# Kernel optimization log

Hardware: AMD Instinct MI355X
Metric: run time of the kernel (lower is better)

Reference implementation:

```python
import jax, jax.numpy as jnp
import numpy as np

BN_EPS = 1e-5
NN_EPS = 1e-8


def _conv_bn_relu(x, w, gamma, beta, mean, var):
    # x: (B, Cin, N), w: (Cout, Cin) -- 1x1 Conv1d (no bias) + BatchNorm1d (eval) + ReLU
    y = jnp.einsum('oc,bcn->bon', w, x)
    scale = gamma / jnp.sqrt(var + BN_EPS)            # (Cout,)
    shift = beta - mean * scale                       # (Cout,)
    return jax.nn.relu(y * scale[:, None] + shift[:, None])


def setup_inputs() -> dict:
    key = jax.random.key(0)
    ks = jax.random.split(key, 10)
    B, N, M = 4, 2048, 8192
    Cin, Cout = 512, 256
    inp = {
        'x1': jax.random.normal(ks[0], (B, Cin, N), dtype=jnp.float32),
        'p1': jax.random.uniform(ks[1], (B, N, 3), dtype=jnp.float32) * 4.0,
        'x2': jax.random.normal(ks[2], (B, Cout, M), dtype=jnp.float32),
        'p2': jax.random.uniform(ks[3], (B, M, 3), dtype=jnp.float32) * 4.0,
        # up_mlp params
        'w_up': jax.random.normal(ks[4], (Cout, Cin), dtype=jnp.float32) * (1.0 / np.sqrt(Cin)),
        'g_up': jnp.ones((Cout,), jnp.float32),
        'b_up': jnp.zeros((Cout,), jnp.float32),
        'm_up': jax.random.normal(ks[5], (Cout,), dtype=jnp.float32) * 0.1,
        'v_up': jax.random.uniform(ks[6], (Cout,), dtype=jnp.float32) + 0.5,
        # lateral_mlp params
        'w_lat': jax.random.normal(ks[7], (Cout, Cout), dtype=jnp.float32) * (1.0 / np.sqrt(Cout)),
        'g_lat': jnp.ones((Cout,), jnp.float32),
        'b_lat': jnp.zeros((Cout,), jnp.float32),
        'm_lat': jax.random.normal(ks[8], (Cout,), dtype=jnp.float32) * 0.1,
        'v_lat': jax.random.uniform(ks[9], (Cout,), dtype=jnp.float32) + 0.5,
    }
    return inp


def reference(x1, p1, x2, p2, w_up, g_up, b_up, m_up, v_up,
              w_lat, g_lat, b_lat, m_lat, v_lat):
    # up branch: conv1x1 + BN + ReLU on coarse features  (B, Cout, N)
    f1 = _conv_bn_relu(x1, w_up, g_up, b_up, m_up, v_up)

    # three_nn: for each fine point p2 find 3 nearest coarse points p1 (squared dist)
    d2 = (jnp.sum(p2 * p2, -1)[:, :, None]
          + jnp.sum(p1 * p1, -1)[:, None, :]
          - 2.0 * jnp.einsum('bmd,bnd->bmn', p2, p1))        # (B, M, N)
    d2 = jnp.maximum(d2, 0.0)
    neg_d, idx = jax.lax.top_k(-d2, 3)                       # (B, M, 3)
    dist = -neg_d

    # inverse-distance weights
    dist_recip = 1.0 / (dist + NN_EPS)
    weight = dist_recip / jnp.sum(dist_recip, axis=2, keepdims=True)  # (B, M, 3)

    # three_interpolate: gather + weighted sum
    gathered = jax.vmap(lambda f, i: f[:, i])(f1, idx)       # (B, Cout, M, 3)
    interp = jnp.einsum('bcmk,bmk->bcm', gathered, weight)   # (B, Cout, M)

    # lateral branch
    f2 = _conv_bn_relu(x2, w_lat, g_lat, b_lat, m_lat, v_lat)

    return interp + f2, p2
```

## Files before the change

kernel.cpp:

```cpp
#include <hip/hip_runtime.h>
#include <math.h>
#include <float.h>

#define B_    4
#define N_    2048
#define M_    8192
#define CIN_  512
#define COUT_ 256

typedef __attribute__((ext_vector_type(8))) short short8v;
typedef __attribute__((ext_vector_type(4))) float f32x4;

__device__ __forceinline__ void ws_store_f32(float* p, float v) {
    __hip_atomic_store((unsigned int*)p, __float_as_uint(v),
                       __ATOMIC_RELAXED, __HIP_MEMORY_SCOPE_SYSTEM);
}
__device__ __forceinline__ void ws_store_u32(int* p, int v) {
    __hip_atomic_store((unsigned int*)p, (unsigned int)v,
                       __ATOMIC_RELAXED, __HIP_MEMORY_SCOPE_SYSTEM);
}
__device__ __forceinline__ void l2_invalidate() {
    asm volatile("buffer_inv sc0 sc1" ::: "memory");
}

__device__ __forceinline__ unsigned short f2bf(float f) {
    unsigned u = __float_as_uint(f);
    u += 0x7fffu + ((u >> 16) & 1u);
    return (unsigned short)(u >> 16);
}

template<int K, int MODE>
__device__ __forceinline__ void gemm_body(
    char* raw, int b, int c0, int m0,
    const float* __restrict__ X, const float* __restrict__ W,
    const float* __restrict__ gam, const float* __restrict__ bet,
    const float* __restrict__ mu, const float* __restrict__ var,
    float* __restrict__ dst,
    const float* __restrict__ f1t, const int* __restrict__ nn_idx,
    const float* __restrict__ nn_w, int Mdim)
{
    char* Ab = raw;
    char* Bb = raw + 10240;

    const int tid = threadIdx.x;
    const int l  = tid & 63;
    const int wv = tid >> 6;
    const int wc = wv & 1, wn = wv >> 1;

    f32x4 acc[4][4];
    #pragma unroll
    for (int i = 0; i < 4; ++i)
        #pragma unroll
        for (int j = 0; j < 4; ++j)
            acc[i][j] = (f32x4){0.f, 0.f, 0.f, 0.f};

    const int ksA = tid & 7;
    const int crA = tid >> 3;
    const int kqB = tid >> 5;
    const int mlB = tid & 31;

    for (int kc = 0; kc < K; kc += 32) {
        #pragma unroll
        for (int r = 0; r < 4; ++r) {
            int c = crA + 32 * r;
            float4 v = *(const float4*)(W + (size_t)(c0 + c) * K + kc + ksA * 4);
            unsigned lo = f2bf(v.x) | ((unsigned)f2bf(v.y) << 16);
            unsigned hi = f2bf(v.z) | ((unsigned)f2bf(v.w) << 16);
            *(uint2*)(Ab + c * 80 + ksA * 8) = make_uint2(lo, hi);
        }
        #pragma unroll
        for (int jj = 0; jj < 4; ++jj) {
            int m = mlB + 32 * jj;
            const float* xp = X + ((size_t)b * K + kc + kqB * 4) * Mdim + m0 + m;
            float v0 = xp[0];
            float v1 = xp[(size_t)Mdim];
            float v2 = xp[(size_t)2 * Mdim];
            float v3 = xp[(size_t)3 * Mdim];
            unsigned lo = f2bf(v0) | ((unsigned)f2bf(v1) << 16);
            unsigned hi = f2bf(v2) | ((unsigned)f2bf(v3) << 16);
            *(uint2*)(Bb + m * 80 + kqB * 8) = make_uint2(lo, hi);
        }
        __syncthreads();
        short8v a[4], bf[4];
        #pragma unroll
        for (int ci = 0; ci < 4; ++ci)
            a[ci] = *(const short8v*)(Ab + (wc * 64 + ci * 16 + (l & 15)) * 80 + (l >> 4) * 16);
        #pragma unroll
        for (int ni = 0; ni < 4; ++ni)
            bf[ni] = *(const short8v*)(Bb + (wn * 64 + ni * 16 + (l & 15)) * 80 + (l >> 4) * 16);
        #pragma unroll
        for (int ci = 0; ci < 4; ++ci)
            #pragma unroll
            for (int ni = 0; ni < 4; ++ni)
                acc[ci][ni] = __builtin_amdgcn_mfma_f32_16x16x32_bf16(
                    a[ci], bf[ni], acc[ci][ni], 0, 0, 0);
        __syncthreads();
    }

    const int lc = (l >> 4) * 4;
    float scA[4][4], shA[4][4];
    #pragma unroll
    for (int ci = 0; ci < 4; ++ci)
        #pragma unroll
        for (int r = 0; r < 4; ++r) {
            int c = c0 + wc * 64 + ci * 16 + lc + r;
            float sc = gam[c] / sqrtf(var[c] + 1e-5f);
            scA[ci][r] = sc;
            shA[ci][r] = bet[c] - mu[c] * sc;
        }

    if constexpr (MODE == 0) {
        float* S = (float*)raw;
        #pragma unroll
        for (int h = 0; h < 2; ++h) {
            if (wn == h) {
                #pragma unroll
                for (int ni = 0; ni < 4; ++ni)
                    #pragma unroll
                    for (int ci = 0; ci < 4; ++ci)
                        #pragma unroll
                        for (int r = 0; r < 4; ++r)
                            S[(ni * 16 + (l & 15)) * 133 + wc * 64 + ci * 16 + lc + r] =
                                fmaxf(acc[ci][ni][r] * scA[ci][r] + shA[ci][r], 0.f);
            }
            __syncthreads();
            #pragma unroll
            for (int i = 0; i < 32; ++i) {
                int e = tid + i * 256;
                int row = e >> 7, c = e & 127;
                ws_store_f32(dst + ((size_t)b * N_ + m0 + h * 64 + row) * COUT_ + c0 + c,
                             S[row * 133 + c]);
            }
            __syncthreads();
        }
    } else {
        #pragma unroll
        for (int ni = 0; ni < 4; ++ni) {
            int mg = m0 + wn * 64 + ni * 16 + (l & 15);
            size_t io = ((size_t)b * M_ + mg) * 3;
            int   i0 = nn_idx[io + 0];
            int   i1 = nn_idx[io + 1];
            int   i2 = nn_idx[io + 2];
            float w0 = nn_w[io + 0];
            float w1 = nn_w[io + 1];
            float w2 = nn_w[io + 2];
            const float4* g0 = (const float4*)(f1t + ((size_t)b * N_ + i0) * COUT_ + c0 + wc * 64 + lc);
            const float4* g1 = (const float4*)(f1t + ((size_t)b * N_ + i1) * COUT_ + c0 + wc * 64 + lc);
            const float4* g2 = (const float4*)(f1t + ((size_t)b * N_ + i2) * COUT_ + c0 + wc * 64 + lc);
            #pragma unroll
            for (int ci = 0; ci < 4; ++ci) {
                float4 G0 = g0[ci * 4];
                float4 G1 = g1[ci * 4];
                float4 G2 = g2[ci * 4];
                const float* f0 = (const float*)&G0;
                const float* f1 = (const float*)&G1;
                const float* f2 = (const float*)&G2;
                #pragma unroll
                for (int r = 0; r < 4; ++r) {
                    float v = fmaxf(acc[ci][ni][r] * scA[ci][r] + shA[ci][r], 0.f);
                    v = fmaf(w0, f0[r], v);
                    v = fmaf(w1, f1[r], v);
                    v = fmaf(w2, f2[r], v);
                    int c = c0 + wc * 64 + ci * 16 + lc + r;
                    dst[((size_t)b * COUT_ + c) * M_ + mg] = v;
                }
            }
        }
    }
}

__device__ __forceinline__ void lex_insert(float e, int j,
    float& D0, float& D1, float& D2, int& I0, int& I1, int& I2)
{
    bool l0 = (e < D0) || (e == D0 && j < I0);
    bool l1 = (e < D1) || (e == D1 && j < I1);
    bool l2 = (e < D2) || (e == D2 && j < I2);
    if (l2) {
        if (l0)      { D2=D1; I2=I1; D1=D0; I1=I0; D0=e; I0=j; }
        else if (l1) { D2=D1; I2=I1; D1=e;  I1=j; }
        else         { D2=e;  I2=j; }
    }
}

__device__ __forceinline__ void bubble_insert(float e, int ie,
    float& D0, float& D1, float& D2, int& I0, int& I1, int& I2)
{
    bool l2 = e < D2;
    D2 = l2 ? e  : D2;
    I2 = l2 ? ie : I2;
    bool s1 = D2 < D1;
    float tf = D1; int ti = I1;
    D1 = s1 ? D2 : D1;  I1 = s1 ? I2 : I1;
    D2 = s1 ? tf : D2;  I2 = s1 ? ti : I2;
    bool s0 = D1 < D0;
    tf = D0; ti = I0;
    D0 = s0 ? D1 : D0;  I0 = s0 ? I1 : I0;
    D1 = s0 ? tf : D1;  I1 = s0 ? ti : I1;
}

__device__ __forceinline__ void three_nn_body(
    float4 (*P)[257], int b, int mb,
    const float* __restrict__ p1, const float* __restrict__ p2,
    int* __restrict__ nn_idx, float* __restrict__ nn_w,
    float* __restrict__ out1)
{
    #pragma unroll
    for (int r = 0; r < 8; ++r) {
        int n = r * 256 + threadIdx.x;
        float x = p1[((size_t)(b*N_)+n)*3 + 0];
        float y = p1[((size_t)(b*N_)+n)*3 + 1];
        float z = p1[((size_t)(b*N_)+n)*3 + 2];
        float t = x * x;
        t = fmaf(y, y, t);
        t = fmaf(z, z, t);
        P[r][threadIdx.x] = make_float4(x, y, z, t);
    }
    __syncthreads();

    const int m = mb * 32 + (threadIdx.x >> 3);
    const int s = threadIdx.x & 7;
    const size_t pbase = ((size_t)(b*M_) + m) * 3;
    const float qx = p2[pbase+0], qy = p2[pbase+1], qz = p2[pbase+2];
    float s2 = qx * qx;
    s2 = fmaf(qy, qy, s2);
    s2 = fmaf(qz, qz, s2);

    float D0 = FLT_MAX, D1 = FLT_MAX, D2 = FLT_MAX;
    int   I0 = 0x7fffffff, I1 = 0x7fffffff, I2 = 0x7fffffff;
    const int base = s * 256;
    const float4* Ps = &P[s][0];

    for (int t = 0; t < 256; t += 8) {
        float4 c[8];
        #pragma unroll
        for (int u = 0; u < 8; ++u) c[u] = Ps[t + u];
        float d[8];
        #pragma unroll
        for (int u = 0; u < 8; ++u) {
            float dot = qx * c[u].x;
            dot = fmaf(qy, c[u].y, dot);
            dot = fmaf(qz, c[u].z, dot);
            float d2 = fmaf(-2.0f, dot, s2 + c[u].w);
            d[u] = fmaxf(d2, 0.0f);
        }
        #pragma unroll
        for (int u = 0; u < 8; ++u)
            bubble_insert(d[u], base + t + u, D0, D1, D2, I0, I1, I2);
    }

    #pragma unroll
    for (int st = 1; st <= 4; st <<= 1) {
        float E0 = __shfl_xor(D0, st), E1 = __shfl_xor(D1, st), E2 = __shfl_xor(D2, st);
        int   J0 = __shfl_xor(I0, st), J1 = __shfl_xor(I1, st), J2 = __shfl_xor(I2, st);
        lex_insert(E0, J0, D0, D1, D2, I0, I1, I2);
        lex_insert(E1, J1, D0, D1, D2, I0, I1, I2);
        lex_insert(E2, J2, D0, D1, D2, I0, I1, I2);
    }
    if (s == 0) {
        float r0 = 1.0f / (D0 + 1e-8f);
        float r1 = 1.0f / (D1 + 1e-8f);
        float r2 = 1.0f / (D2 + 1e-8f);
        float sum = (r0 + r1) + r2;
        size_t o = ((size_t)(b*M_) + m) * 3;
        ws_store_u32(nn_idx + o+0, I0);
        ws_store_u32(nn_idx + o+1, I1);
        ws_store_u32(nn_idx + o+2, I2);
        ws_store_f32(nn_w + o+0, r0 / sum);
        ws_store_f32(nn_w + o+1, r1 / sum);
        ws_store_f32(nn_w + o+2, r2 / sum);
        out1[o+0] = qx; out1[o+1] = qy; out1[o+2] = qz;
    }
}

__global__ __launch_bounds__(256) void up_nn_kernel(
    const float* __restrict__ x1, const float* __restrict__ w_up,
    const float* __restrict__ g_up, const float* __restrict__ b_up,
    const float* __restrict__ m_up, const float* __restrict__ v_up,
    float* __restrict__ f1t,
    const float* __restrict__ p1, const float* __restrict__ p2,
    int* __restrict__ nn_idx, float* __restrict__ nn_w,
    float* __restrict__ out1)
{
    __shared__ float4 raw4[2130];
    int bid = blockIdx.x;
    if (bid < 128) {
        int nb = bid & 15, cb = (bid >> 4) & 1, b = bid >> 5;
        gemm_body<CIN_, 0>((char*)raw4, b, cb * 128, nb * 128,
                           x1, w_up, g_up, b_up, m_up, v_up, f1t,
                           nullptr, nullptr, nullptr, N_);
    } else {
        int v = bid - 128;
        int mb = v & 255, b = v >> 8;
        three_nn_body((float4(*)[257])raw4, b, mb, p1, p2, nn_idx, nn_w, out1);
    }
}

__global__ __launch_bounds__(256) void lat_kernel(
    const float* __restrict__ x2, const float* __restrict__ w_lat,
    const float* __restrict__ g_lat, const float* __restrict__ b_lat,
    const float* __restrict__ m_lat, const float* __restrict__ v_lat,
    const float* __restrict__ f1t, const int* __restrict__ nn_idx,
    const float* __restrict__ nn_w, float* __restrict__ out0)
{
    __shared__ float4 raw4[1280];
    l2_invalidate();
    gemm_body<COUT_, 1>((char*)raw4, blockIdx.z, blockIdx.y * 128, blockIdx.x * 128,
                        x2, w_lat, g_lat, b_lat, m_lat, v_lat, out0,
                        f1t, nn_idx, nn_w, M_);
}

extern "C" void kernel_launch(void* const* d_in, const int* in_sizes, int n_in,
                              void* d_out, int out_size, void* d_ws, size_t ws_size,
                              hipStream_t stream)
{
    (void)in_sizes; (void)n_in; (void)out_size; (void)ws_size;

    const float* x1    = (const float*)d_in[0];
    const float* p1    = (const float*)d_in[1];
    const float* x2    = (const float*)d_in[2];
    const float* p2    = (const float*)d_in[3];
    const float* w_up  = (const float*)d_in[4];
    const float* g_up  = (const float*)d_in[5];
    const float* b_up  = (const float*)d_in[6];
    const float* m_up  = (const float*)d_in[7];
    const float* v_up  = (const float*)d_in[8];
    const float* w_lat = (const float*)d_in[9];
    const float* g_lat = (const float*)d_in[10];
    const float* b_lat = (const float*)d_in[11];
    const float* m_lat = (const float*)d_in[12];
    const float* v_lat = (const float*)d_in[13];

    float* out0 = (float*)d_out;
    float* out1 = out0 + (size_t)B_ * COUT_ * M_;

    float* f1t   = (float*)d_ws;
    int*   nn_idx = (int*)((char*)d_ws + (size_t)B_ * N_ * COUT_ * 4);
    float* nn_w   = (float*)((char*)nn_idx + (size_t)B_ * M_ * 3 * 4);

    up_nn_kernel<<<dim3(128 + 1024), 256, 0, stream>>>(
        x1, w_up, g_up, b_up, m_up, v_up, f1t, p1, p2, nn_idx, nn_w, out1);

    lat_kernel<<<dim3(M_ / 128, COUT_ / 128, B_), 256, 0, stream>>>(
        x2, w_lat, g_lat, b_lat, m_lat, v_lat, f1t, nn_idx, nn_w, out0);
}
```

Baseline: 115.4 us.

## Split fused up/NN kernel, prefetch GEMM tiles in registers, pack NN records

Splits the fused up-projection plus three_nn kernel into separate launches and adds a dedicated cache-invalidate kernel in place of the per-block invalidate in lat_kernel. The GEMM body now loads the next K-slice into registers while the current one is converted and stored to shared memory, to hide global load latency. The three_nn inner loop double-buffers LDS reads. Neighbor indices and weights are packed into one 8-float record per point, so the lateral kernel fetches them with two vector loads. The extra launches add overhead and remove the overlap that the fused kernel had between the GEMM and the NN search.

```diff
diff --git a/kernel.cpp b/kernel.cpp
--- a/kernel.cpp
+++ b/kernel.cpp
@@ -19,7 +19,8 @@
     __hip_atomic_store((unsigned int*)p, (unsigned int)v,
                        __ATOMIC_RELAXED, __HIP_MEMORY_SCOPE_SYSTEM);
 }
-__device__ __forceinline__ void l2_invalidate() {
+
+__global__ __launch_bounds__(64) void inv_kernel() {
     asm volatile("buffer_inv sc0 sc1" ::: "memory");
 }
 
@@ -36,8 +37,7 @@
     const float* __restrict__ gam, const float* __restrict__ bet,
     const float* __restrict__ mu, const float* __restrict__ var,
     float* __restrict__ dst,
-    const float* __restrict__ f1t, const int* __restrict__ nn_idx,
-    const float* __restrict__ nn_w, int Mdim)
+    const float* __restrict__ f1t, const float* __restrict__ nnrec, int Mdim)
 {
     char* Ab = raw;
     char* Bb = raw + 10240;
@@ -59,41 +59,60 @@
     const int kqB = tid >> 5;
     const int mlB = tid & 31;
 
+    float4 wreg[4];
+    float  xreg[4][4];
+    #pragma unroll
+    for (int r = 0; r < 4; ++r)
+        wreg[r] = *(const float4*)(W + (size_t)(c0 + crA + 32 * r) * K + ksA * 4);
+    #pragma unroll
+    for (int jj = 0; jj < 4; ++jj) {
+        const float* xp = X + ((size_t)b * K + kqB * 4) * Mdim + m0 + mlB + 32 * jj;
+        xreg[jj][0] = xp[0];
+        xreg[jj][1] = xp[(size_t)Mdim];
+        xreg[jj][2] = xp[(size_t)2 * Mdim];
+        xreg[jj][3] = xp[(size_t)3 * Mdim];
+    }
+
     for (int kc = 0; kc < K; kc += 32) {
         #pragma unroll
         for (int r = 0; r < 4; ++r) {
-            int c = crA + 32 * r;
-            float4 v = *(const float4*)(W + (size_t)(c0 + c) * K + kc + ksA * 4);
-            unsigned lo = f2bf(v.x) | ((unsigned)f2bf(v.y) << 16);
-            unsigned hi = f2bf(v.z) | ((unsigned)f2bf(v.w) << 16);
-            *(uint2*)(Ab + c * 80 + ksA * 8) = make_uint2(lo, hi);
+            unsigned lo = f2bf(wreg[r].x) | ((unsigned)f2bf(wreg[r].y) << 16);
+            unsigned hi = f2bf(wreg[r].z) | ((unsigned)f2bf(wreg[r].w) << 16);
+            *(uint2*)(Ab + (crA + 32 * r) * 80 + ksA * 8) = make_uint2(lo, hi);
         }
         #pragma unroll
         for (int jj = 0; jj < 4; ++jj) {
-            int m = mlB + 32 * jj;
-            const float* xp = X + ((size_t)b * K + kc + kqB * 4) * Mdim + m0 + m;
-            float v0 = xp[0];
-            float v1 = xp[(size_t)Mdim];
-            float v2 = xp[(size_t)2 * Mdim];
-            float v3 = xp[(size_t)3 * Mdim];
-            unsigned lo = f2bf(v0) | ((unsigned)f2bf(v1) << 16);
-            unsigned hi = f2bf(v2) | ((unsigned)f2bf(v3) << 16);
-            *(uint2*)(Bb + m * 80 + kqB * 8) = make_uint2(lo, hi);
+            unsigned lo = f2bf(xreg[jj][0]) | ((unsigned)f2bf(xreg[jj][1]) << 16);
+            unsigned hi = f2bf(xreg[jj][2]) | ((unsigned)f2bf(xreg[jj][3]) << 16);
+            *(uint2*)(Bb + (mlB + 32 * jj) * 80 + kqB * 8) = make_uint2(lo, hi);
+        }
+        if (kc + 32 < K) {
+            #pragma unroll
+            for (int r = 0; r < 4; ++r)
+                wreg[r] = *(const float4*)(W + (size_t)(c0 + crA + 32 * r) * K + (kc + 32) + ksA * 4);
+            #pragma unroll
+            for (int jj = 0; jj < 4; ++jj) {
+                const float* xp = X + ((size_t)b * K + (kc + 32) + kqB * 4) * Mdim + m0 + mlB + 32 * jj;
+                xreg[jj][0] = xp[0];
+                xreg[jj][1] = xp[(size_t)Mdim];
+                xreg[jj][2] = xp[(size_t)2 * Mdim];
+                xreg[jj][3] = xp[(size_t)3 * Mdim];
+            }
         }
         __syncthreads();
-        short8v a[4], bf[4];
+        short8v a[4], bfv[4];
         #pragma unroll
         for (int ci = 0; ci < 4; ++ci)
             a[ci] = *(const short8v*)(Ab + (wc * 64 + ci * 16 + (l & 15)) * 80 + (l >> 4) * 16);
         #pragma unroll
         for (int ni = 0; ni < 4; ++ni)
-            bf[ni] = *(const short8v*)(Bb + (wn * 64 + ni * 16 + (l & 15)) * 80 + (l >> 4) * 16);
+            bfv[ni] = *(const short8v*)(Bb + (wn * 64 + ni * 16 + (l & 15)) * 80 + (l >> 4) * 16);
         #pragma unroll
         for (int ci = 0; ci < 4; ++ci)
             #pragma unroll
             for (int ni = 0; ni < 4; ++ni)
                 acc[ci][ni] = __builtin_amdgcn_mfma_f32_16x16x32_bf16(
-                    a[ci], bf[ni], acc[ci][ni], 0, 0, 0);
+                    a[ci], bfv[ni], acc[ci][ni], 0, 0, 0);
         __syncthreads();
     }
 
@@ -137,13 +156,13 @@
         #pragma unroll
         for (int ni = 0; ni < 4; ++ni) {
             int mg = m0 + wn * 64 + ni * 16 + (l & 15);
-            size_t io = ((size_t)b * M_ + mg) * 3;
-            int   i0 = nn_idx[io + 0];
-            int   i1 = nn_idx[io + 1];
-            int   i2 = nn_idx[io + 2];
-            float w0 = nn_w[io + 0];
-            float w1 = nn_w[io + 1];
-            float w2 = nn_w[io + 2];
+            const float* rp = nnrec + ((size_t)b * M_ + mg) * 8;
+            float4 ra = *(const float4*)rp;
+            float2 rb = *(const float2*)(rp + 4);
+            int   i0 = __float_as_int(ra.x);
+            int   i1 = __float_as_int(ra.y);
+            int   i2 = __float_as_int(ra.z);
+            float w0 = ra.w, w1 = rb.x, w2 = rb.y;
             const float4* g0 = (const float4*)(f1t + ((size_t)b * N_ + i0) * COUT_ + c0 + wc * 64 + lc);
             const float4* g1 = (const float4*)(f1t + ((size_t)b * N_ + i1) * COUT_ + c0 + wc * 64 + lc);
             const float4* g2 = (const float4*)(f1t + ((size_t)b * N_ + i2) * COUT_ + c0 + wc * 64 + lc);
@@ -169,6 +188,31 @@
     }
 }
 
+__global__ __launch_bounds__(256) void up_kernel(
+    const float* __restrict__ x1, const float* __restrict__ w_up,
+    const float* __restrict__ g_up, const float* __restrict__ b_up,
+    const float* __restrict__ m_up, const float* __restrict__ v_up,
+    float* __restrict__ f1t)
+{
+    __shared__ float4 raw4[2130];
+    gemm_body<CIN_, 0>((char*)raw4, blockIdx.z, blockIdx.y * 128, blockIdx.x * 128,
+                       x1, w_up, g_up, b_up, m_up, v_up, f1t,
+                       nullptr, nullptr, N_);
+}
+
+__global__ __launch_bounds__(256) void lat_kernel(
+    const float* __restrict__ x2, const float* __restrict__ w_lat,
+    const float* __restrict__ g_lat, const float* __restrict__ b_lat,
+    const float* __restrict__ m_lat, const float* __restrict__ v_lat,
+    const float* __restrict__ f1t, const float* __restrict__ nnrec,
+    float* __restrict__ out0)
+{
+    __shared__ float4 raw4[1280];
+    gemm_body<COUT_, 1>((char*)raw4, blockIdx.z, blockIdx.y * 128, blockIdx.x * 128,
+                        x2, w_lat, g_lat, b_lat, m_lat, v_lat, out0,
+                        f1t, nnrec, M_);
+}
+
 __device__ __forceinline__ void lex_insert(float e, int j,
     float& D0, float& D1, float& D2, int& I0, int& I1, int& I2)
 {
@@ -198,12 +242,12 @@
     D1 = s0 ? tf : D1;  I1 = s0 ? ti : I1;
 }
 
-__device__ __forceinline__ void three_nn_body(
-    float4 (*P)[257], int b, int mb,
+__global__ __launch_bounds__(256) void three_nn_kernel(
     const float* __restrict__ p1, const float* __restrict__ p2,
-    int* __restrict__ nn_idx, float* __restrict__ nn_w,
-    float* __restrict__ out1)
-{
+    float* __restrict__ nnrec, float* __restrict__ out1)
+{
+    __shared__ float4 P[8][257];
+    const int b = blockIdx.y;
     #pragma unroll
     for (int r = 0; r < 8; ++r) {
         int n = r * 256 + threadIdx.x;
@@ -217,7 +261,7 @@
     }
     __syncthreads();
 
-    const int m = mb * 32 + (threadIdx.x >> 3);
+    const int m = blockIdx.x * 32 + (threadIdx.x >> 3);
     const int s = threadIdx.x & 7;
     const size_t pbase = ((size_t)(b*M_) + m) * 3;
     const float qx = p2[pbase+0], qy = p2[pbase+1], qz = p2[pbase+2];
@@ -230,23 +274,37 @@
     const int base = s * 256;
     const float4* Ps = &P[s][0];
 
-    for (int t = 0; t < 256; t += 8) {
-        float4 c[8];
-        #pragma unroll
-        for (int u = 0; u < 8; ++u) c[u] = Ps[t + u];
-        float d[8];
-        #pragma unroll
-        for (int u = 0; u < 8; ++u) {
-            float dot = qx * c[u].x;
-            dot = fmaf(qy, c[u].y, dot);
-            dot = fmaf(qz, c[u].z, dot);
-            float d2 = fmaf(-2.0f, dot, s2 + c[u].w);
-            d[u] = fmaxf(d2, 0.0f);
-        }
-        #pragma unroll
-        for (int u = 0; u < 8; ++u)
-            bubble_insert(d[u], base + t + u, D0, D1, D2, I0, I1, I2);
-    }
+    float4 ca[8], cb[8];
+    #pragma unroll
+    for (int u = 0; u < 8; ++u) ca[u] = Ps[u];
+
+    #define PROC(CV, IB)                                                     \
+        {                                                                    \
+            float d[8];                                                      \
+            _Pragma("unroll")                                                \
+            for (int u = 0; u < 8; ++u) {                                    \
+                float dot = qx * CV[u].x;                                    \
+                dot = fmaf(qy, CV[u].y, dot);                                \
+                dot = fmaf(qz, CV[u].z, dot);                                \
+                float d2 = fmaf(-2.0f, dot, s2 + CV[u].w);                   \
+                d[u] = fmaxf(d2, 0.0f);                                      \
+            }                                                                \
+            _Pragma("unroll")                                                \
+            for (int u = 0; u < 8; ++u)                                      \
+                bubble_insert(d[u], (IB) + u, D0, D1, D2, I0, I1, I2);       \
+        }
+
+    for (int j = 0; j < 32; j += 2) {
+        #pragma unroll
+        for (int u = 0; u < 8; ++u) cb[u] = Ps[(j + 1) * 8 + u];
+        PROC(ca, base + j * 8);
+        if (j + 2 < 32) {
+            #pragma unroll
+            for (int u = 0; u < 8; ++u) ca[u] = Ps[(j + 2) * 8 + u];
+        }
+        PROC(cb, base + (j + 1) * 8);
+    }
+    #undef PROC
 
     #pragma unroll
     for (int st = 1; st <= 4; st <<= 1) {
@@ -261,52 +319,16 @@
         float r1 = 1.0f / (D1 + 1e-8f);
         float r2 = 1.0f / (D2 + 1e-8f);
         float sum = (r0 + r1) + r2;
+        float* rp = nnrec + ((size_t)(b*M_) + m) * 8;
+        ws_store_u32((int*)rp + 0, I0);
+        ws_store_u32((int*)rp + 1, I1);
+        ws_store_u32((int*)rp + 2, I2);
+        ws_store_f32(rp + 3, r0 / sum);
+        ws_store_f32(rp + 4, r1 / sum);
+        ws_store_f32(rp + 5, r2 / sum);
         size_t o = ((size_t)(b*M_) + m) * 3;
-        ws_store_u32(nn_idx + o+0, I0);
-        ws_store_u32(nn_idx + o+1, I1);
-        ws_store_u32(nn_idx + o+2, I2);
-        ws_store_f32(nn_w + o+0, r0 / sum);
-        ws_store_f32(nn_w + o+1, r1 / sum);
-        ws_store_f32(nn_w + o+2, r2 / sum);
         out1[o+0] = qx; out1[o+1] = qy; out1[o+2] = qz;
     }
-}
-
-__global__ __launch_bounds__(256) void up_nn_kernel(
-    const float* __restrict__ x1, const float* __restrict__ w_up,
-    const float* __restrict__ g_up, const float* __restrict__ b_up,
-    const float* __restrict__ m_up, const float* __restrict__ v_up,
-    float* __restrict__ f1t,
-    const float* __restrict__ p1, const float* __restrict__ p2,
-    int* __restrict__ nn_idx, float* __restrict__ nn_w,
-    float* __restrict__ out1)
-{
-    __shared__ float4 raw4[2130];
-    int bid = blockIdx.x;
-    if (bid < 128) {
-        int nb = bid & 15, cb = (bid >> 4) & 1, b = bid >> 5;
-        gemm_body<CIN_, 0>((char*)raw4, b, cb * 128, nb * 128,
-                           x1, w_up, g_up, b_up, m_up, v_up, f1t,
-                           nullptr, nullptr, nullptr, N_);
-    } else {
-        int v = bid - 128;
-        int mb = v & 255, b = v >> 8;
-        three_nn_body((float4(*)[257])raw4, b, mb, p1, p2, nn_idx, nn_w, out1);
-    }
-}
-
-__global__ __launch_bounds__(256) void lat_kernel(
-    const float* __restrict__ x2, const float* __restrict__ w_lat,
-    const float* __restrict__ g_lat, const float* __restrict__ b_lat,
-    const float* __restrict__ m_lat, const float* __restrict__ v_lat,
-    const float* __restrict__ f1t, const int* __restrict__ nn_idx,
-    const float* __restrict__ nn_w, float* __restrict__ out0)
-{
-    __shared__ float4 raw4[1280];
-    l2_invalidate();
-    gemm_body<COUT_, 1>((char*)raw4, blockIdx.z, blockIdx.y * 128, blockIdx.x * 128,
-                        x2, w_lat, g_lat, b_lat, m_lat, v_lat, out0,
-                        f1t, nn_idx, nn_w, M_);
 }
 
 extern "C" void kernel_launch(void* const* d_in, const int* in_sizes, int n_in,
@@ -334,12 +356,16 @@
     float* out1 = out0 + (size_t)B_ * COUT_ * M_;
 
     float* f1t   = (float*)d_ws;
-    int*   nn_idx = (int*)((char*)d_ws + (size_t)B_ * N_ * COUT_ * 4);
-    float* nn_w   = (float*)((char*)nn_idx + (size_t)B_ * M_ * 3 * 4);
-
-    up_nn_kernel<<<dim3(128 + 1024), 256, 0, stream>>>(
-        x1, w_up, g_up, b_up, m_up, v_up, f1t, p1, p2, nn_idx, nn_w, out1);
+    float* nnrec = (float*)((char*)d_ws + (size_t)B_ * N_ * COUT_ * 4);
+
+    up_kernel<<<dim3(N_ / 128, COUT_ / 128, B_), 256, 0, stream>>>(
+        x1, w_up, g_up, b_up, m_up, v_up, f1t);
+
+    three_nn_kernel<<<dim3(M_ / 32, B_), 256, 0, stream>>>(
+        p1, p2, nnrec, out1);
+
+    inv_kernel<<<dim3(512), 64, 0, stream>>>();
 
     lat_kernel<<<dim3(M_ / 128, COUT_ / 128, B_), 256, 0, stream>>>(
-        x2, w_lat, g_lat, b_lat, m_lat, v_lat, f1t, nn_idx, nn_w, out0);
-}
+        x2, w_lat, g_lat, b_lat, m_lat, v_lat, f1t, nnrec, out0);
+}
```

Measured after the change: 103.4 us. 10.4% less time.
